# Kernel optimization log

Hardware: AMD Instinct MI355X
Metric: run time of the kernel (lower is better)

## Reference

```python
import jax, jax.numpy as jnp
import numpy as np

H, B, N, D = 8, 256, 200, 128
KD = D // H                      # key_dim = embed_dim // n_heads = 16
TRI = N * (N - 1) // 2           # strictly upper-triangular count per matrix
NORM = 1.0 / np.sqrt(KD)
NEG = -jnp.inf


def setup_inputs() -> dict:
    key = jax.random.key(0)
    k1, k2, k3, k4, k5 = jax.random.split(key, 5)
    q = jax.random.normal(k1, (B, N, D), dtype=jnp.float32)
    che_mask = jax.random.randint(k2, (H, B, TRI), 0, 2).astype(bool)
    exchange = jax.random.randint(k3, (B, 2), 0, N)
    stdv = 1.0 / np.sqrt(KD)
    Wq = jax.random.uniform(k4, (H, D, KD), jnp.float32, -stdv, stdv)
    Wk = jax.random.uniform(k5, (H, D, KD), jnp.float32, -stdv, stdv)
    return {"q": q, "che_mask": che_mask, "exchange": exchange, "Wq": Wq, "Wk": Wk}


def reference(q, che_mask, exchange, Wq, Wk):
    # Q, K: (H, B, N, KD)
    Q = jnp.einsum('bnd,hdk->hbnk', q, Wq)
    K = jnp.einsum('bnd,hdk->hbnk', q, Wk)
    # tanh-rescaled scores: (H, B, N, N)
    comp = jnp.tanh(NORM * jnp.einsum('hbik,hbjk->hbij', Q, K)) * 10.0

    # 1) lower triangle (incl. diagonal) -> -inf
    tril = jnp.tril(jnp.ones((N, N), dtype=bool))
    comp = jnp.where(tril, NEG, comp)

    # 2) strictly-upper positions where che_mask == 0 -> -inf
    # torch boolean indexing enumerates ~tril elements row-major == triu_indices order
    iu0, iu1 = np.triu_indices(N, k=1)
    keep = jnp.zeros((H, B, N, N), dtype=bool).at[:, :, iu0, iu1].set(che_mask)
    comp = jnp.where(jnp.logical_and(~tril, ~keep), NEG, comp)

    # 3) last 28 query rows fully masked
    comp = comp.at[:, :, -28:, :].set(NEG)

    # 4) per-batch exchange-pair scatter on head 0 only
    b_idx = jnp.arange(B)
    comp = comp.at[0, b_idx, exchange[:, 1], exchange[:, 0]].set(NEG)
    comp = comp.at[0, b_idx, exchange[:, 0], exchange[:, 1]].set(NEG)

    # 5) fixed column 100 masked
    comp = comp.at[:, :, :, 100].set(NEG)

    # global (flattened over N*N) softmax / log_softmax per (head, batch)
    im = comp.reshape(H, B, N * N)
    return jax.nn.log_softmax(im, axis=-1), jax.nn.softmax(im, axis=-1)
```

## Files before the change

### kernel.cpp

```cpp
#include <hip/hip_runtime.h>
#include <math.h>

#define Hh 8
#define Bb 256
#define Nn 200
#define Dd 128
#define KDk 16
#define TRI_ 19900
#define NN_ 40000
#define OUT_HALF 81920000ull
#define QK_FLOATS 6553600

#define NEG_FIN (-1.0e30f)

#define NITEMS 385
#define NWAVES 16
#define ITEMS_PER_WAVE 25

__device__ __forceinline__ float fast_exp2(float x) {
#if __has_builtin(__builtin_amdgcn_exp2f)
  return __builtin_amdgcn_exp2f(x);
#else
  return exp2f(x);
#endif
}
__device__ __forceinline__ float fast_log2(float x) {
#if __has_builtin(__builtin_amdgcn_logf)
  return __builtin_amdgcn_logf(x);
#else
  return log2f(x);
#endif
}
__device__ __forceinline__ float fast_rcp(float x) {
#if __has_builtin(__builtin_amdgcn_rcpf)
  return __builtin_amdgcn_rcpf(x);
#else
  return 1.0f / x;
#endif
}

__device__ __forceinline__ float dot16(float4 a0, float4 a1, float4 a2, float4 a3,
                                       float4 b0, float4 b1, float4 b2, float4 b3) {
  return a0.x*b0.x + a0.y*b0.y + a0.z*b0.z + a0.w*b0.w
       + a1.x*b1.x + a1.y*b1.y + a1.z*b1.z + a1.w*b1.w
       + a2.x*b2.x + a2.y*b2.y + a2.z*b2.z + a2.w*b2.w
       + a3.x*b3.x + a3.y*b3.y + a3.z*b3.z + a3.w*b3.w;
}

struct ItemTab { unsigned int v[NWAVES * ITEMS_PER_WAVE]; };
static constexpr ItemTab make_tab() {
  ItemTab t{};
  int n = 0;
  for (int i = 0; i < 172; ++i) {
    int len = 199 - i;
    int g = (len + 63) >> 6;
    for (int k = 0; k < g; ++k) { t.v[n] = (unsigned int)((i << 2) | k); ++n; }
  }
  for (; n < NWAVES * ITEMS_PER_WAVE; ++n) t.v[n] = 0xFFFFu;
  return t;
}
__constant__ ItemTab d_tab = make_tab();

__global__ void k_detect(const unsigned char* __restrict__ che, int* __restrict__ flag) {
  const int t = threadIdx.x;
  unsigned char a4 = 0, a8 = 0;
  #pragma unroll
  for (int k = 0; k < 16; ++k) {
    const int i = t * 16 + k;
    const unsigned char v = che[i];
    if (i & 3) a4 |= v;
    else if (i & 7) a8 |= v;
  }
  const unsigned long long m4 = __ballot(a4 != 0);
  const unsigned long long m8 = __ballot(a8 != 0);
  if (t == 0) *flag = m4 ? 1 : (m8 ? 4 : 8);
}

__global__ __launch_bounds__(256) void k_proj(const float* __restrict__ q,
    const float* __restrict__ Wq, const float* __restrict__ Wk,
    float* __restrict__ Qg, float* __restrict__ Kg) {
  __shared__ float As[64 * 132];
  __shared__ float Bst[128 * 68];
  const int tid = threadIdx.x;
  const int r0 = blockIdx.x * 64;
  const int c0 = blockIdx.y * 64;

  const float4* src = (const float4*)q;
  #pragma unroll
  for (int p = 0; p < 8; ++p) {
    const int t2 = tid + p * 256;
    const int row = t2 >> 5, q4 = t2 & 31;
    float4 v = src[(size_t)(r0 + row) * 32 + q4];
    *(float4*)&As[row * 132 + q4 * 4] = v;
  }
  #pragma unroll
  for (int p = 0; p < 32; ++p) {
    const int t2 = tid + p * 256;
    const int d = t2 >> 6, cl = t2 & 63;
    const int c = c0 + cl;
    const int h = c >> 5, m = (c >> 4) & 1, kk = c & 15;
    const float* Wsrc = m ? Wk : Wq;
    Bst[d * 68 + cl] = Wsrc[(h * 128 + d) * 16 + kk];
  }
  __syncthreads();

  const int tn = tid >> 4;
  const int tc = tid & 15;
  float acc[4][4] = {};
  #pragma unroll
  for (int dq = 0; dq < 32; ++dq) {
    float a[4][4];
    #pragma unroll
    for (int r = 0; r < 4; ++r) {
      float4 t = *(const float4*)&As[(tn * 4 + r) * 132 + dq * 4];
      a[r][0] = t.x; a[r][1] = t.y; a[r][2] = t.z; a[r][3] = t.w;
    }
    #pragma unroll
    for (int dd = 0; dd < 4; ++dd) {
      float4 bv = *(const float4*)&Bst[(dq * 4 + dd) * 68 + tc * 4];
      #pragma unroll
      for (int r = 0; r < 4; ++r) {
        acc[r][0] += a[r][dd] * bv.x;
        acc[r][1] += a[r][dd] * bv.y;
        acc[r][2] += a[r][dd] * bv.z;
        acc[r][3] += a[r][dd] * bv.w;
      }
    }
  }
  const int cq = c0 + tc * 4;
  const int h = cq >> 5, m = (cq >> 4) & 1, kkb = cq & 15;
  float* dst = m ? Kg : Qg;
  #pragma unroll
  for (int r = 0; r < 4; ++r) {
    const int nrow = r0 + tn * 4 + r;
    const int b = nrow / 200, n = nrow - b * 200;
    float4 v = make_float4(acc[r][0], acc[r][1], acc[r][2], acc[r][3]);
    *(float4*)(dst + (size_t)((h * 256 + b) * 200 + n) * 16 + kkb) = v;
  }
}

__global__ __launch_bounds__(1024, 4) void k_attn(
    const float* __restrict__ Qg, const float* __restrict__ Kg,
    const unsigned char* __restrict__ che, const int* __restrict__ exch,
    const int* __restrict__ flag, float* __restrict__ out) {
  const int hb = blockIdx.x;
  const int h = hb >> 8, b = hb & 255;
  const int tid = threadIdx.x;
  const int lane = tid & 63;
  const int wave = __builtin_amdgcn_readfirstlane(tid >> 6);
  const float* __restrict__ Qb = Qg + (size_t)hb * 3200;
  const float* __restrict__ Kb = Kg + (size_t)hb * 3200;
  const int cs = *flag;
  const unsigned char* __restrict__ cheB = che + (size_t)hb * (size_t)TRI_ * (size_t)cs;
  const int e0 = exch[2 * b], e1 = exch[2 * b + 1];
  const int emin = min(e0, e1), emax = max(e0, e1);
  const bool h0 = (h == 0);

  __shared__ float red[NWAVES];

  const float C2E = 0.72134752044448f;
  const float L2E = 1.44269504088896f;

  float sreg[ITEMS_PER_WAVE];
  float psum = 0.0f;

  #pragma unroll
  for (int s = 0; s < ITEMS_PER_WAVE; ++s) {
    const int iv = (int)d_tab.v[wave * ITEMS_PER_WAVE + s];
    const int i = iv >> 2;
    const int g = iv & 3;
    const int ic = (i < 172) ? i : 0;
    const int j = i + 1 + (g << 6) + lane;
    const int jc = (j < 200) ? j : 0;
    int live = ((j < 200) & (j != 100) & (i < 172)) ? 1 : 0;
    const int base = ic * 199 - ((ic * (ic - 1)) >> 1) - ic - 1;
    const int idx = live ? (base + j) : 0;
    live &= (cheB[(size_t)idx * (size_t)cs] != 0) ? 1 : 0;
    if (h0 && (i == emin) && (j == emax)) live = 0;
    const float4* kp = (const float4*)(Kb + jc * 16);
    const float4 k0 = kp[0], k1 = kp[1], k2 = kp[2], k3 = kp[3];
    const float4* qp = (const float4*)(Qb + ic * 16);
    const float d = dot16(qp[0], qp[1], qp[2], qp[3], k0, k1, k2, k3);
    const float E = fast_exp2(C2E * d);
    const float rc = fast_rcp(E + 1.0f);
    const float s10 = live ? (-20.0f * rc) : NEG_FIN;
    psum += fast_exp2(L2E * s10);
    sreg[s] = s10;
  }

  #pragma unroll
  for (int o = 32; o > 0; o >>= 1) psum += __shfl_xor(psum, o, 64);
  if (lane == 0) red[wave] = psum;
  __syncthreads();
  float Z = 0.0f;
  #pragma unroll
  for (int w2 = 0; w2 < NWAVES; ++w2) Z += red[w2];
  const float lnZ = 0.69314718056f * fast_log2(Z);

  const size_t obase = (size_t)hb * NN_;
  float* __restrict__ oLS = out + obase;
  float* __restrict__ oSM = out + OUT_HALF + obase;

  #pragma unroll
  for (int s = 0; s < ITEMS_PER_WAVE; ++s) {
    const int iv = (int)d_tab.v[wave * ITEMS_PER_WAVE + s];
    const int i = iv >> 2;
    const int g = iv & 3;
    const int j = i + 1 + (g << 6) + lane;
    if ((i < 172) && (j < 200)) {
      const float ls = sreg[s] - lnZ;
      const float sm = fast_exp2(L2E * ls);
      const int o = i * 200 + j;
      __builtin_nontemporal_store(ls, &oLS[o]);
      __builtin_nontemporal_store(sm, &oSM[o]);
    }
  }

  for (int r = wave; r < 200; r += NWAVES) {
    const int lim = (r < 172) ? r : 199;
    #pragma unroll
    for (int gc = 0; gc < 4; ++gc) {
      const int j = (gc << 6) + lane;
      if (j <= lim && j < 200) {
        const int o = r * 200 + j;
        __builtin_nontemporal_store(NEG_FIN, &oLS[o]);
        __builtin_nontemporal_store(0.0f, &oSM[o]);
      }
    }
  }
}

extern "C" void kernel_launch(void* const* d_in, const int* in_sizes, int n_in,
                              void* d_out, int out_size, void* d_ws, size_t ws_size,
                              hipStream_t stream) {
  const float* q           = (const float*)d_in[0];
  const unsigned char* che = (const unsigned char*)d_in[1];
  const int* exch          = (const int*)d_in[2];
  const float* Wq          = (const float*)d_in[3];
  const float* Wk          = (const float*)d_in[4];
  float* out = (float*)d_out;
  float* ws  = (float*)d_ws;

  const size_t need = (size_t)(4 + 2 * QK_FLOATS) * sizeof(float);
  int* flag = (int*)ws;
  float* Qg = ws + 4;
  float* Kg = Qg + QK_FLOATS;

  if (ws_size < need) {
    k_detect<<<dim3(1), dim3(64), 0, stream>>>(che, flag);
    return;
  }

  k_detect<<<dim3(1), dim3(64), 0, stream>>>(che, flag);
  k_proj<<<dim3(800, 4), dim3(256), 0, stream>>>(q, Wq, Wk, Qg, Kg);
  k_attn<<<dim3(2048), dim3(1024), 0, stream>>>(Qg, Kg, che, exch, flag, out);
}
```

Before: 1.081 ms.

## Restructure attention kernel into row-wise recompute with LDS mask and float4 stores

Each block now stages the che_mask bytes for its (head, batch) into shared memory and holds four K rows per lane in registers. Scores are recomputed in the write phase instead of being kept in a per-item register array. Each row is written once with coalesced float4 stores that cover both the triangular and masked regions, replacing the scalar nontemporal stores and the separate fill loop. The cost is doing the dot products and exps twice, using about 20KB of LDS per block, which may limit occupancy, and switching to plain rather than nontemporal stores.

```diff
diff --git a/kernel.cpp b/kernel.cpp
--- a/kernel.cpp
+++ b/kernel.cpp
@@ -13,10 +13,6 @@
 
 #define NEG_FIN (-1.0e30f)
 
-#define NITEMS 385
-#define NWAVES 16
-#define ITEMS_PER_WAVE 25
-
 __device__ __forceinline__ float fast_exp2(float x) {
 #if __has_builtin(__builtin_amdgcn_exp2f)
   return __builtin_amdgcn_exp2f(x);
@@ -46,20 +42,6 @@
        + a2.x*b2.x + a2.y*b2.y + a2.z*b2.z + a2.w*b2.w
        + a3.x*b3.x + a3.y*b3.y + a3.z*b3.z + a3.w*b3.w;
 }
-
-struct ItemTab { unsigned int v[NWAVES * ITEMS_PER_WAVE]; };
-static constexpr ItemTab make_tab() {
-  ItemTab t{};
-  int n = 0;
-  for (int i = 0; i < 172; ++i) {
-    int len = 199 - i;
-    int g = (len + 63) >> 6;
-    for (int k = 0; k < g; ++k) { t.v[n] = (unsigned int)((i << 2) | k); ++n; }
-  }
-  for (; n < NWAVES * ITEMS_PER_WAVE; ++n) t.v[n] = 0xFFFFu;
-  return t;
-}
-__constant__ ItemTab d_tab = make_tab();
 
 __global__ void k_detect(const unsigned char* __restrict__ che, int* __restrict__ flag) {
   const int t = threadIdx.x;
@@ -156,36 +138,45 @@
   const int emin = min(e0, e1), emax = max(e0, e1);
   const bool h0 = (h == 0);
 
-  __shared__ float red[NWAVES];
+  __shared__ float red[16];
+  __shared__ unsigned char cheS[TRI_ + 4];
 
   const float C2E = 0.72134752044448f;
   const float L2E = 1.44269504088896f;
 
-  float sreg[ITEMS_PER_WAVE];
+  for (int o = tid; o < TRI_; o += 1024) cheS[o] = cheB[(size_t)o * (size_t)cs];
+
+  const int kq = (lane < 50) ? lane : 49;
+  float4 kr[4][4];
+  #pragma unroll
+  for (int c = 0; c < 4; ++c) {
+    const float4* kp = (const float4*)(Kb + (size_t)(4 * kq + c) * 16);
+    kr[c][0] = kp[0]; kr[c][1] = kp[1]; kr[c][2] = kp[2]; kr[c][3] = kp[3];
+  }
+  __syncthreads();
+
   float psum = 0.0f;
-
-  #pragma unroll
-  for (int s = 0; s < ITEMS_PER_WAVE; ++s) {
-    const int iv = (int)d_tab.v[wave * ITEMS_PER_WAVE + s];
-    const int i = iv >> 2;
-    const int g = iv & 3;
-    const int ic = (i < 172) ? i : 0;
-    const int j = i + 1 + (g << 6) + lane;
-    const int jc = (j < 200) ? j : 0;
-    int live = ((j < 200) & (j != 100) & (i < 172)) ? 1 : 0;
-    const int base = ic * 199 - ((ic * (ic - 1)) >> 1) - ic - 1;
-    const int idx = live ? (base + j) : 0;
-    live &= (cheB[(size_t)idx * (size_t)cs] != 0) ? 1 : 0;
-    if (h0 && (i == emin) && (j == emax)) live = 0;
-    const float4* kp = (const float4*)(Kb + jc * 16);
-    const float4 k0 = kp[0], k1 = kp[1], k2 = kp[2], k3 = kp[3];
-    const float4* qp = (const float4*)(Qb + ic * 16);
-    const float d = dot16(qp[0], qp[1], qp[2], qp[3], k0, k1, k2, k3);
-    const float E = fast_exp2(C2E * d);
-    const float rc = fast_rcp(E + 1.0f);
-    const float s10 = live ? (-20.0f * rc) : NEG_FIN;
-    psum += fast_exp2(L2E * s10);
-    sreg[s] = s10;
+  const int ntB = (wave < 12) ? 11 : 10;
+  #pragma unroll 1
+  for (int t = 0; t < ntB; ++t) {
+    const int r = wave + 16 * t;
+    const int base = r * 199 - ((r * (r - 1)) >> 1) - r - 1;
+    const float4* qp = (const float4*)(Qb + (size_t)r * 16);
+    const float4 q0 = qp[0], q1 = qp[1], q2 = qp[2], q3 = qp[3];
+    if (lane < 50 && 4 * lane + 3 > r) {
+      #pragma unroll
+      for (int c = 0; c < 4; ++c) {
+        const int j = 4 * lane + c;
+        int live = ((j > r) & (j != 100)) ? 1 : 0;
+        const int idx = live ? (base + j) : 0;
+        live &= (cheS[idx] != 0) ? 1 : 0;
+        if (h0 && (r == emin) && (j == emax)) live = 0;
+        const float d = dot16(q0, q1, q2, q3, kr[c][0], kr[c][1], kr[c][2], kr[c][3]);
+        const float E = fast_exp2(C2E * d);
+        const float s10 = -20.0f * fast_rcp(E + 1.0f);
+        psum += live ? fast_exp2(L2E * s10) : 0.0f;
+      }
+    }
   }
 
   #pragma unroll
@@ -194,38 +185,43 @@
   __syncthreads();
   float Z = 0.0f;
   #pragma unroll
-  for (int w2 = 0; w2 < NWAVES; ++w2) Z += red[w2];
+  for (int w2 = 0; w2 < 16; ++w2) Z += red[w2];
   const float lnZ = 0.69314718056f * fast_log2(Z);
 
   const size_t obase = (size_t)hb * NN_;
   float* __restrict__ oLS = out + obase;
   float* __restrict__ oSM = out + OUT_HALF + obase;
 
-  #pragma unroll
-  for (int s = 0; s < ITEMS_PER_WAVE; ++s) {
-    const int iv = (int)d_tab.v[wave * ITEMS_PER_WAVE + s];
-    const int i = iv >> 2;
-    const int g = iv & 3;
-    const int j = i + 1 + (g << 6) + lane;
-    if ((i < 172) && (j < 200)) {
-      const float ls = sreg[s] - lnZ;
-      const float sm = fast_exp2(L2E * ls);
-      const int o = i * 200 + j;
-      __builtin_nontemporal_store(ls, &oLS[o]);
-      __builtin_nontemporal_store(sm, &oSM[o]);
-    }
-  }
-
-  for (int r = wave; r < 200; r += NWAVES) {
-    const int lim = (r < 172) ? r : 199;
+  const int ntC = (wave < 8) ? 13 : 12;
+  #pragma unroll 1
+  for (int t = 0; t < ntC; ++t) {
+    const int r = wave + 16 * t;
+    float lsv[4], smv[4];
     #pragma unroll
-    for (int gc = 0; gc < 4; ++gc) {
-      const int j = (gc << 6) + lane;
-      if (j <= lim && j < 200) {
-        const int o = r * 200 + j;
-        __builtin_nontemporal_store(NEG_FIN, &oLS[o]);
-        __builtin_nontemporal_store(0.0f, &oSM[o]);
+    for (int c = 0; c < 4; ++c) { lsv[c] = NEG_FIN; smv[c] = 0.0f; }
+    if (r < 172 && lane < 50 && 4 * lane + 3 > r) {
+      const int base = r * 199 - ((r * (r - 1)) >> 1) - r - 1;
+      const float4* qp = (const float4*)(Qb + (size_t)r * 16);
+      const float4 q0 = qp[0], q1 = qp[1], q2 = qp[2], q3 = qp[3];
+      #pragma unroll
+      for (int c = 0; c < 4; ++c) {
+        const int j = 4 * lane + c;
+        int live = ((j > r) & (j != 100)) ? 1 : 0;
+        const int idx = live ? (base + j) : 0;
+        live &= (cheS[idx] != 0) ? 1 : 0;
+        if (h0 && (r == emin) && (j == emax)) live = 0;
+        const float d = dot16(q0, q1, q2, q3, kr[c][0], kr[c][1], kr[c][2], kr[c][3]);
+        const float E = fast_exp2(C2E * d);
+        const float s10 = -20.0f * fast_rcp(E + 1.0f);
+        const float ls = s10 - lnZ;
+        lsv[c] = live ? ls : NEG_FIN;
+        smv[c] = live ? fast_exp2(L2E * ls) : 0.0f;
       }
+    }
+    if (lane < 50) {
+      const size_t ro = (size_t)r * 200;
+      *(float4*)(oLS + ro + 4 * lane) = make_float4(lsv[0], lsv[1], lsv[2], lsv[3]);
+      *(float4*)(oSM + ro + 4 * lane) = make_float4(smv[0], smv[1], smv[2], smv[3]);
     }
   }
 }
```

After: 957.5 us. 1.13x faster.
